# Kernel tuning notes

Hardware: AMD Instinct MI355X
Metric: run time of the kernel (lower is better)

Reference implementation:

```python
import jax, jax.numpy as jnp
import numpy as np

SEGMENT_LENGTHS = [2048, 4096, 8192]
DILATION_RATES = [1, 2, 4]
EPS = 1e-8


def setup_inputs() -> dict:
    key = jax.random.key(0)
    kq, kk, kv = jax.random.split(key, 3)
    shape = (4, 8192, 8, 64)  # (b, n, h, d)
    return {
        "query": jax.random.normal(kq, shape, dtype=jnp.float32),
        "key": jax.random.normal(kk, shape, dtype=jnp.float32),
        "value": jax.random.normal(kv, shape, dtype=jnp.float32),
    }


def _dilated_attention(query, key, value):
    b, n, h, d = query.shape
    ng = len(SEGMENT_LENGTHS)
    group_sizes = [h // ng] * ng
    for i in range(h % ng):
        group_sizes[i] += 1
    scale = 1.0 / (d ** 0.5)  # torch SDPA default: 1/sqrt(E), E = last dim

    out = jnp.zeros_like(query)
    for i, (g, r, s) in enumerate(zip(group_sizes, DILATION_RATES, SEGMENT_LENGTHS)):
        offset = i % r
        hmin = sum(group_sizes[:i])
        hmax = hmin + g
        nseg = n // s
        # (b, nseg, s, h, d) -> strided dilation slice + head-group slice
        qg = query.reshape(b, nseg, s, h, d)[:, :, offset::r, hmin:hmax, :]
        kg = key.reshape(b, nseg, s, h, d)[:, :, offset::r, hmin:hmax, :]
        vg = value.reshape(b, nseg, s, h, d)[:, :, offset::r, hmin:hmax, :]
        # Faithful to the torch code: SDPA is fed (bn, s, h, d) untransposed, so
        # attention is over the HEAD axis (length g); s is a batch-like axis.
        scores = jnp.einsum('bnsqd,bnskd->bnsqk', qg, kg) * scale  # (b,nseg,sd,g,g)
        attn = jax.nn.softmax(scores, axis=-1)
        x = jnp.einsum('bnsqk,bnskd->bnsqd', attn, vg)  # (b,nseg,sd,g,d)
        # custom sum-normalization over (segment, dilated-position) dims
        x = x / (x.sum(axis=(1, 2), keepdims=True) + EPS)
        # scatter-add back into the strided/head-sliced locations
        out = (out.reshape(b, nseg, s, h, d)
                  .at[:, :, offset::r, hmin:hmax, :].add(x)
                  .reshape(b, n, h, d))
    return out / ng


def reference(query, key, value):
    return _dilated_attention(query, key, value)
```

## Files before the change

### kernel.cpp

```cpp
#include <hip/hip_runtime.h>
#include <math.h>

#define NB 4
#define NN 8192
#define NH 8
#define ND 64
#define NPART_STRIDE 192
#define N_BLOCKS_P1 3584


__device__ __forceinline__ void gload_lds16(const float* g, float* l) {
    __builtin_amdgcn_global_load_lds(
        (__attribute__((address_space(1))) void*)const_cast<float*>(g),
        (__attribute__((address_space(3))) void*)l, 16, 0, 0);
}

template<int G>
__device__ __forceinline__ void pass1_work(
    const float* __restrict__ Q, const float* __restrict__ K,
    const float* __restrict__ V, float* __restrict__ out,
    float* __restrict__ partials,
    float (*stage)[9][256], float (*red)[3][64],
    int b, int chunk, int r, int off, int hmin, int seglen)
{
    const int tid  = threadIdx.x;
    const int w    = tid >> 6;
    const int lane = tid & 63;
    const int sg   = lane >> 4;
    const int l    = lane & 15;

    const int j   = chunk * 16 + w * 4 + sg;
    const int pos = (j >> 11) * seglen + off + (j & 2047) * r;
    const size_t rowbase = (((size_t)b * NN + pos) * NH + hmin) * ND + 4 * l;

    #pragma unroll
    for (int q = 0; q < G; ++q) gload_lds16(Q + rowbase + q * ND, &stage[w][q][0]);
    #pragma unroll
    for (int q = 0; q < G; ++q) gload_lds16(K + rowbase + q * ND, &stage[w][3 + q][0]);
    #pragma unroll
    for (int q = 0; q < G; ++q) gload_lds16(V + rowbase + q * ND, &stage[w][6 + q][0]);

    asm volatile("s_waitcnt vmcnt(%0)" :: "n"(G) : "memory");
    __builtin_amdgcn_sched_barrier(0);

    float4 qv[G], kv[G];
    #pragma unroll
    for (int q = 0; q < G; ++q) {
        qv[q] = *(const float4*)&stage[w][q][4 * lane];
        kv[q] = *(const float4*)&stage[w][3 + q][4 * lane];
    }

    float sc[G][G];
    #pragma unroll
    for (int q = 0; q < G; ++q)
        #pragma unroll
        for (int k = 0; k < G; ++k)
            sc[q][k] = qv[q].x * kv[k].x + qv[q].y * kv[k].y
                     + qv[q].z * kv[k].z + qv[q].w * kv[k].w;

    #pragma unroll
    for (int o = 8; o >= 1; o >>= 1)
        #pragma unroll
        for (int q = 0; q < G; ++q)
            #pragma unroll
            for (int k = 0; k < G; ++k)
                sc[q][k] += __shfl_xor(sc[q][k], o);

    #pragma unroll
    for (int q = 0; q < G; ++q) {
        float m = -INFINITY;
        #pragma unroll
        for (int k = 0; k < G; ++k) { sc[q][k] *= 0.125f; m = fmaxf(m, sc[q][k]); }
        float ssum = 0.f;
        #pragma unroll
        for (int k = 0; k < G; ++k) { sc[q][k] = __expf(sc[q][k] - m); ssum += sc[q][k]; }
        const float rs = 1.f / ssum;
        #pragma unroll
        for (int k = 0; k < G; ++k) sc[q][k] *= rs;
    }

    asm volatile("s_waitcnt vmcnt(0)" ::: "memory");
    __builtin_amdgcn_sched_barrier(0);

    float4 vv[G];
    #pragma unroll
    for (int q = 0; q < G; ++q)
        vv[q] = *(const float4*)&stage[w][6 + q][4 * lane];

    float xs[G][4];
    #pragma unroll
    for (int q = 0; q < G; ++q) {
        float xe0 = 0.f, xe1 = 0.f, xe2 = 0.f, xe3 = 0.f;
        #pragma unroll
        for (int k = 0; k < G; ++k) {
            const float aw = sc[q][k];
            xe0 += aw * vv[k].x; xe1 += aw * vv[k].y;
            xe2 += aw * vv[k].z; xe3 += aw * vv[k].w;
        }
        *(float4*)(out + rowbase + (size_t)q * ND) = make_float4(xe0, xe1, xe2, xe3);
        xs[q][0] = xe0; xs[q][1] = xe1; xs[q][2] = xe2; xs[q][3] = xe3;
    }

    #pragma unroll
    for (int q = 0; q < G; ++q)
        #pragma unroll
        for (int e = 0; e < 4; ++e) {
            xs[q][e] += __shfl_xor(xs[q][e], 16);
            xs[q][e] += __shfl_xor(xs[q][e], 32);
        }

    if (lane < 16)
        #pragma unroll
        for (int q = 0; q < G; ++q)
            *(float4*)&red[w][q][4 * l] = make_float4(xs[q][0], xs[q][1], xs[q][2], xs[q][3]);
    __syncthreads();

    if (tid < G * 64) {
        const int q = tid >> 6;
        const int d = tid & 63;
        partials[(size_t)blockIdx.x * NPART_STRIDE + q * 64 + d] =
            red[0][q][d] + red[1][q][d] + red[2][q][d] + red[3][q][d];
    }
}

__global__ __launch_bounds__(256)
void sda_pass1(const float* __restrict__ Q, const float* __restrict__ K,
               const float* __restrict__ V, float* __restrict__ out,
               float* __restrict__ partials)
{
    __shared__ float stage[4][9][256];
    __shared__ float red[4][3][64];
    const int bid = blockIdx.x;
    if (bid < 2048) {
        const int b = bid >> 9, chunk = bid & 511;
        pass1_work<3>(Q, K, V, out, partials, stage, red, b, chunk, 1, 0, 0, 2048);
    } else if (bid < 3072) {
        const int loc = bid - 2048;
        const int b = loc >> 8, chunk = loc & 255;
        pass1_work<3>(Q, K, V, out, partials, stage, red, b, chunk, 2, 1, 3, 4096);
    } else {
        const int loc = bid - 3072;
        const int b = loc >> 7, chunk = loc & 127;
        pass1_work<2>(Q, K, V, out, partials, stage, red, b, chunk, 4, 2, 6, 8192);
    }
}

__global__ __launch_bounds__(256)
void sda_pass2a(const float* __restrict__ partials, float* __restrict__ partial2)
{
    const int bid   = blockIdx.x;
    const int bh    = bid >> 3;
    const int slice = bid & 7;
    const int b     = bh >> 3;
    const int h     = bh & 7;
    const int d     = threadIdx.x & 63;
    const int part  = threadIdx.x >> 6;
    int qi, bstart, cnt;
    if (h < 3)      { qi = h;     bstart = b * 512;        cnt = 512; }
    else if (h < 6) { qi = h - 3; bstart = 2048 + b * 256; cnt = 256; }
    else            { qi = h - 6; bstart = 3072 + b * 128; cnt = 128; }
    const int len = cnt >> 3;
    const int c0  = bstart + slice * len;
    float s = 0.f;
    #pragma unroll 4
    for (int c = part; c < len; c += 4)
        s += partials[(size_t)(c0 + c) * NPART_STRIDE + qi * 64 + d];
    __shared__ float sred[4][64];
    sred[part][d] = s;
    __syncthreads();
    if (part == 0)
        partial2[(size_t)bid * 64 + d] = sred[0][d] + sred[1][d] + sred[2][d] + sred[3][d];
}

__global__ __launch_bounds__(256)
void sda_pass2b(const float* __restrict__ partial2, float* __restrict__ inv)
{
    const int t = blockIdx.x * 256 + threadIdx.x;
    if (t >= NB * NH * ND) return;
    const int bh = t >> 6;
    const int d  = t & 63;
    float s = 0.f;
    #pragma unroll
    for (int sl = 0; sl < 8; ++sl)
        s += partial2[(size_t)(bh * 8 + sl) * 64 + d];
    inv[t] = 1.f / (3.f * (s + 1e-8f));
}

__global__ __launch_bounds__(256)
void sda_pass3(float* __restrict__ out, const float* __restrict__ inv)
{
    const int total4 = NB * NN * NH * ND / 4;
    for (int idx = blockIdx.x * 256 + threadIdx.x; idx < total4;
         idx += gridDim.x * 256) {
        const int d4  = idx & 15;
        const int rem = idx >> 4;
        const int h   = rem & 7;
        const int pos = (rem >> 3) & 8191;
        const int b   = rem >> 16;
        const bool cov = (h < 3) || ((h < 6) ? ((pos & 1) == 1) : ((pos & 3) == 2));
        float4 o;
        if (cov) {
            const float4 v = ((const float4*)out)[idx];
            const float4 f = ((const float4*)inv)[b * 128 + h * 16 + d4];
            o = make_float4(v.x * f.x, v.y * f.y, v.z * f.z, v.w * f.w);
        } else {
            o = make_float4(0.f, 0.f, 0.f, 0.f);
        }
        ((float4*)out)[idx] = o;
    }
}

extern "C" void kernel_launch(void* const* d_in, const int* in_sizes, int n_in,
                              void* d_out, int out_size, void* d_ws, size_t ws_size,
                              hipStream_t stream)
{
    const float* Q = (const float*)d_in[0];
    const float* K = (const float*)d_in[1];
    const float* V = (const float*)d_in[2];
    float* out      = (float*)d_out;
    float* partials = (float*)d_ws;
    float* partial2 = partials + (size_t)N_BLOCKS_P1 * NPART_STRIDE;
    float* inv      = partial2 + 256 * 64;

    hipLaunchKernelGGL(sda_pass1,  dim3(N_BLOCKS_P1), dim3(256), 0, stream,
                       Q, K, V, out, partials);
    hipLaunchKernelGGL(sda_pass2a, dim3(256), dim3(256), 0, stream, partials, partial2);
    hipLaunchKernelGGL(sda_pass2b, dim3(8),   dim3(256), 0, stream, partial2, inv);
    hipLaunchKernelGGL(sda_pass3,  dim3(2048), dim3(256), 0, stream, out, inv);
}
```

Measured before the change: 53.26 us.

## Make pass1 waves persistent over 8 tasks with double-buffered LDS prefetch

Pass1 now launches 448 blocks instead of 3584. Each wave handles 8 consecutive tasks, loading the next task's Q/K/V into a second LDS buffer while it computes the current one. Per-wave partial sums accumulate in registers and are written straight to the partials buffer without the block-level LDS reduction and __syncthreads, and pass2a's indexing is updated to match. The goal is to hide global-load latency and cut block launch and sync overhead, at the cost of doubled LDS use per block (lower occupancy) and fewer blocks to spread across CUs.

```diff
diff --git a/kernel.cpp b/kernel.cpp
--- a/kernel.cpp
+++ b/kernel.cpp
@@ -6,7 +6,9 @@
 #define NH 8
 #define ND 64
 #define NPART_STRIDE 192
-#define N_BLOCKS_P1 3584
+#define N_BLOCKS_P1 448
+#define N_WAVES_P1  (N_BLOCKS_P1 * 4)
+#define TASKS 8
 
 
 __device__ __forceinline__ void gload_lds16(const float* g, float* l) {
@@ -16,38 +18,38 @@
 }
 
 template<int G>
-__device__ __forceinline__ void pass1_work(
+__device__ __forceinline__ size_t task_rowbase(
+    int wave_local, int t, int sg, int l,
+    int b, int r, int off, int seglen, int hmin)
+{
+    const int j   = (wave_local * TASKS + t) * 4 + sg;
+    const int pos = (j >> 11) * seglen + off + (j & 2047) * r;
+    return (((size_t)b * NN + pos) * NH + hmin) * ND + 4 * l;
+}
+
+template<int G>
+__device__ __forceinline__ void issue_task(
     const float* __restrict__ Q, const float* __restrict__ K,
-    const float* __restrict__ V, float* __restrict__ out,
-    float* __restrict__ partials,
-    float (*stage)[9][256], float (*red)[3][64],
-    int b, int chunk, int r, int off, int hmin, int seglen)
-{
-    const int tid  = threadIdx.x;
-    const int w    = tid >> 6;
-    const int lane = tid & 63;
-    const int sg   = lane >> 4;
-    const int l    = lane & 15;
-
-    const int j   = chunk * 16 + w * 4 + sg;
-    const int pos = (j >> 11) * seglen + off + (j & 2047) * r;
-    const size_t rowbase = (((size_t)b * NN + pos) * NH + hmin) * ND + 4 * l;
-
-    #pragma unroll
-    for (int q = 0; q < G; ++q) gload_lds16(Q + rowbase + q * ND, &stage[w][q][0]);
-    #pragma unroll
-    for (int q = 0; q < G; ++q) gload_lds16(K + rowbase + q * ND, &stage[w][3 + q][0]);
-    #pragma unroll
-    for (int q = 0; q < G; ++q) gload_lds16(V + rowbase + q * ND, &stage[w][6 + q][0]);
-
-    asm volatile("s_waitcnt vmcnt(%0)" :: "n"(G) : "memory");
-    __builtin_amdgcn_sched_barrier(0);
-
+    const float* __restrict__ V, float* buf, size_t rowbase)
+{
+    #pragma unroll
+    for (int q = 0; q < G; ++q) gload_lds16(Q + rowbase + q * ND, buf + q * 256);
+    #pragma unroll
+    for (int q = 0; q < G; ++q) gload_lds16(K + rowbase + q * ND, buf + (G + q) * 256);
+    #pragma unroll
+    for (int q = 0; q < G; ++q) gload_lds16(V + rowbase + q * ND, buf + (2 * G + q) * 256);
+}
+
+template<int G>
+__device__ __forceinline__ void compute_task(
+    const float* buf, float* __restrict__ out, size_t rowbase,
+    int lane, float xs[][4])
+{
     float4 qv[G], kv[G];
     #pragma unroll
     for (int q = 0; q < G; ++q) {
-        qv[q] = *(const float4*)&stage[w][q][4 * lane];
-        kv[q] = *(const float4*)&stage[w][3 + q][4 * lane];
+        qv[q] = *(const float4*)(buf + q * 256 + 4 * lane);
+        kv[q] = *(const float4*)(buf + (G + q) * 256 + 4 * lane);
     }
 
     float sc[G][G];
@@ -79,15 +81,11 @@
         for (int k = 0; k < G; ++k) sc[q][k] *= rs;
     }
 
-    asm volatile("s_waitcnt vmcnt(0)" ::: "memory");
-    __builtin_amdgcn_sched_barrier(0);
-
     float4 vv[G];
     #pragma unroll
     for (int q = 0; q < G; ++q)
-        vv[q] = *(const float4*)&stage[w][6 + q][4 * lane];
-
-    float xs[G][4];
+        vv[q] = *(const float4*)(buf + (2 * G + q) * 256 + 4 * lane);
+
     #pragma unroll
     for (int q = 0; q < G; ++q) {
         float xe0 = 0.f, xe1 = 0.f, xe2 = 0.f, xe3 = 0.f;
@@ -98,8 +96,49 @@
             xe2 += aw * vv[k].z; xe3 += aw * vv[k].w;
         }
         *(float4*)(out + rowbase + (size_t)q * ND) = make_float4(xe0, xe1, xe2, xe3);
-        xs[q][0] = xe0; xs[q][1] = xe1; xs[q][2] = xe2; xs[q][3] = xe3;
-    }
+        xs[q][0] += xe0; xs[q][1] += xe1; xs[q][2] += xe2; xs[q][3] += xe3;
+    }
+}
+
+template<int G>
+__device__ __forceinline__ void pass1_work(
+    const float* __restrict__ Q, const float* __restrict__ K,
+    const float* __restrict__ V, float* __restrict__ out,
+    float* __restrict__ partials, float* st ,
+    int b, int block_local, int wid_base,
+    int r, int off, int hmin, int seglen)
+{
+    const int tid  = threadIdx.x;
+    const int w    = tid >> 6;
+    const int lane = tid & 63;
+    const int sg   = lane >> 4;
+    const int l    = lane & 15;
+
+    const int wave_local = block_local * 4 + w;
+
+    float xs[G][4];
+    #pragma unroll
+    for (int q = 0; q < G; ++q)
+        #pragma unroll
+        for (int e = 0; e < 4; ++e) xs[q][e] = 0.f;
+
+    issue_task<G>(Q, K, V, st,
+                  task_rowbase<G>(wave_local, 0, sg, l, b, r, off, seglen, hmin));
+
+    for (int t = 0; t < TASKS - 1; ++t) {
+        issue_task<G>(Q, K, V, st + ((t + 1) & 1) * (9 * 256),
+                      task_rowbase<G>(wave_local, t + 1, sg, l, b, r, off, seglen, hmin));
+        asm volatile("s_waitcnt vmcnt(%0)" :: "i"(3 * G) : "memory");
+        __builtin_amdgcn_sched_barrier(0);
+        compute_task<G>(st + (t & 1) * (9 * 256), out,
+                        task_rowbase<G>(wave_local, t, sg, l, b, r, off, seglen, hmin),
+                        lane, xs);
+    }
+    asm volatile("s_waitcnt vmcnt(0)" ::: "memory");
+    __builtin_amdgcn_sched_barrier(0);
+    compute_task<G>(st + ((TASKS - 1) & 1) * (9 * 256), out,
+                    task_rowbase<G>(wave_local, TASKS - 1, sg, l, b, r, off, seglen, hmin),
+                    lane, xs);
 
     #pragma unroll
     for (int q = 0; q < G; ++q)
@@ -109,17 +148,12 @@
             xs[q][e] += __shfl_xor(xs[q][e], 32);
         }
 
-    if (lane < 16)
+    if (lane < 16) {
+        const int wid = wid_base + w;
         #pragma unroll
         for (int q = 0; q < G; ++q)
-            *(float4*)&red[w][q][4 * l] = make_float4(xs[q][0], xs[q][1], xs[q][2], xs[q][3]);
-    __syncthreads();
-
-    if (tid < G * 64) {
-        const int q = tid >> 6;
-        const int d = tid & 63;
-        partials[(size_t)blockIdx.x * NPART_STRIDE + q * 64 + d] =
-            red[0][q][d] + red[1][q][d] + red[2][q][d] + red[3][q][d];
+            *(float4*)(partials + (size_t)wid * NPART_STRIDE + q * 64 + 4 * l) =
+                make_float4(xs[q][0], xs[q][1], xs[q][2], xs[q][3]);
     }
 }
 
@@ -128,20 +162,23 @@
                const float* __restrict__ V, float* __restrict__ out,
                float* __restrict__ partials)
 {
-    __shared__ float stage[4][9][256];
-    __shared__ float red[4][3][64];
+    __shared__ float stage[4][2][9][256];
+    float* st = &stage[threadIdx.x >> 6][0][0][0];
     const int bid = blockIdx.x;
-    if (bid < 2048) {
-        const int b = bid >> 9, chunk = bid & 511;
-        pass1_work<3>(Q, K, V, out, partials, stage, red, b, chunk, 1, 0, 0, 2048);
-    } else if (bid < 3072) {
-        const int loc = bid - 2048;
-        const int b = loc >> 8, chunk = loc & 255;
-        pass1_work<3>(Q, K, V, out, partials, stage, red, b, chunk, 2, 1, 3, 4096);
+    if (bid < 256) {
+        const int b = bid >> 6, bl = bid & 63;
+        pass1_work<3>(Q, K, V, out, partials, st, b, bl,
+                      (bid) * 4, 1, 0, 0, 2048);
+    } else if (bid < 384) {
+        const int loc = bid - 256;
+        const int b = loc >> 5, bl = loc & 31;
+        pass1_work<3>(Q, K, V, out, partials, st, b, bl,
+                      bid * 4, 2, 1, 3, 4096);
     } else {
-        const int loc = bid - 3072;
-        const int b = loc >> 7, chunk = loc & 127;
-        pass1_work<2>(Q, K, V, out, partials, stage, red, b, chunk, 4, 2, 6, 8192);
+        const int loc = bid - 384;
+        const int b = loc >> 4, bl = loc & 15;
+        pass1_work<2>(Q, K, V, out, partials, st, b, bl,
+                      bid * 4, 4, 2, 6, 8192);
     }
 }
 
@@ -155,12 +192,12 @@
     const int h     = bh & 7;
     const int d     = threadIdx.x & 63;
     const int part  = threadIdx.x >> 6;
-    int qi, bstart, cnt;
-    if (h < 3)      { qi = h;     bstart = b * 512;        cnt = 512; }
-    else if (h < 6) { qi = h - 3; bstart = 2048 + b * 256; cnt = 256; }
-    else            { qi = h - 6; bstart = 3072 + b * 128; cnt = 128; }
+    int qi, wstart, cnt;
+    if (h < 3)      { qi = h;     wstart = b * 256;        cnt = 256; }
+    else if (h < 6) { qi = h - 3; wstart = 1024 + b * 128; cnt = 128; }
+    else            { qi = h - 6; wstart = 1536 + b * 64;  cnt = 64;  }
     const int len = cnt >> 3;
-    const int c0  = bstart + slice * len;
+    const int c0  = wstart + slice * len;
     float s = 0.f;
     #pragma unroll 4
     for (int c = part; c < len; c += 4)
@@ -219,7 +256,7 @@
     const float* V = (const float*)d_in[2];
     float* out      = (float*)d_out;
     float* partials = (float*)d_ws;
-    float* partial2 = partials + (size_t)N_BLOCKS_P1 * NPART_STRIDE;
+    float* partial2 = partials + (size_t)N_WAVES_P1 * NPART_STRIDE;
     float* inv      = partial2 + 256 * 64;
 
     hipLaunchKernelGGL(sda_pass1,  dim3(N_BLOCKS_P1), dim3(256), 0, stream,
```

Result: no change. 53.59 us (+0.6%).
